# Performance work log

Measured on AMD Instinct MI355X. Metric: run time of the kernel, lower is better.

## Reference

```python
import jax, jax.numpy as jnp
import numpy as np

B, N, IN_DIM, HID, OUT_DIM = 16, 1024, 128, 256, 1024
N_LAYERS, SCT_ORDER, GCN_ORDER = 2, 3, 1
TAU, N_ITER, NOISE_SCALE, TANH_SCALE = 0.1, 20, 0.05, 40.0


def _xavier(key, shape):
    # torch xavier_uniform_ on Linear weight [out, in]
    bound = np.sqrt(6.0 / (shape[-1] + shape[-2]))
    return jax.random.uniform(key, shape, jnp.float32, -bound, bound)


def setup_inputs() -> dict:
    key = jax.random.key(0)
    ks = jax.random.split(key, 12)
    L, H = N_LAYERS, HID
    return {
        "X": jax.random.normal(ks[0], (B, N, IN_DIM), jnp.float32),
        "adj": jax.random.uniform(ks[1], (B, N, N), jnp.float32),
        "w_in": _xavier(ks[2], (H, IN_DIM)),
        "b_in": jnp.zeros((H,), jnp.float32),
        "conv_w1": _xavier(ks[3], (L, H, H)),
        "conv_b1": jnp.zeros((L, H), jnp.float32),
        "conv_w2": _xavier(ks[4], (L, H, H)),
        "conv_b2": jnp.zeros((L, H), jnp.float32),
        "conv_a": 0.1 * jax.random.normal(ks[5], (L, 2 * H, 1), jnp.float32),
        "mlp1_w": _xavier(ks[6], (H, H * (1 + L))),
        "mlp1_b": jnp.zeros((H,), jnp.float32),
        "mlp2_w": _xavier(ks[7], (OUT_DIM, H)),
        "mlp2_b": jnp.zeros((OUT_DIM,), jnp.float32),
    }


def leaky(x):
    return jax.nn.leaky_relu(x, 0.01)


def gcn_diffusion(adj, order, X):
    eye = jnp.eye(adj.shape[-1], dtype=adj.dtype)
    A = adj + eye
    dis = A.sum(-1) ** -0.5                      # [B,N]
    A_hat = dis[..., :, None] * A * dis[..., None, :]
    outs, h = [], X
    for _ in range(order):
        h = A_hat @ h
        outs.append(h)
    return outs


def scattering_diffusion(adj, X, order):
    # lazy random walk P = (I + D^{-1} A)/2; wavelets psi_k = P^{2^{k-1}} - P^{2^k}
    Pmat = adj / adj.sum(-1, keepdims=True)

    def applyP(h):
        return 0.5 * (h + Pmat @ h)

    outs = []
    prev = X
    cur = applyP(X)
    outs.append(prev - cur)
    for k in range(2, order + 1):
        nxt = cur
        for _ in range(2 ** (k - 2)):
            nxt = applyP(nxt)
        outs.append(cur - nxt)
        cur = nxt
    return outs


def sct_conv(X, adj, w1, b1, w2, b2, a, moment=1):
    gcn_list = [leaky(g) for g in gcn_diffusion(adj, GCN_ORDER, X)]
    sct_list = [jnp.abs(h) ** moment for h in scattering_diffusion(adj, X, SCT_ORDER)]
    h_all = jnp.stack(gcn_list + sct_list, axis=1)                    # [B,C,N,H]
    x_rep = jnp.broadcast_to(X[:, None], h_all.shape)                 # [B,C,N,H]
    a_in = jnp.concatenate([x_rep, h_all], axis=-1)                   # [B,C,N,2H]
    e = (jax.nn.relu(a_in) @ a)[..., 0]                               # [B,C,N]
    attention = jax.nn.softmax(e + 1e-10, axis=1)[..., None]          # [B,C,N,1]
    h_prime = (attention * h_all).mean(axis=1)                        # [B,N,H]
    h = leaky(h_prime @ w1.T + b1)
    return leaky(h @ w2.T + b2)


def gumbel_sinkhorn(log_alpha, key):
    u = jax.random.uniform(key, log_alpha.shape, log_alpha.dtype)
    noise = -jnp.log(-jnp.log(u + 1e-20) + 1e-20) * NOISE_SCALE
    Z0 = (log_alpha + noise) / TAU

    def step(Z, _):
        Z = Z - jax.scipy.special.logsumexp(Z, axis=-1, keepdims=True)
        Z = Z - jax.scipy.special.logsumexp(Z, axis=-2, keepdims=True)
        return Z, None

    Z, _ = jax.lax.scan(step, Z0, None, length=N_ITER)
    P = jnp.exp(Z)
    P = P / P.sum(-1, keepdims=True)
    P = P / P.sum(-2, keepdims=True)
    return P, Z0


def reference(X, adj, w_in, b_in, conv_w1, conv_b1, conv_w2, conv_b2, conv_a,
              mlp1_w, mlp1_b, mlp2_w, mlp2_b):
    h = X @ w_in.T + b_in                                             # [B,N,H]
    hidden = [h]
    for l in range(N_LAYERS):
        h = sct_conv(h, adj, conv_w1[l], conv_b1[l], conv_w2[l], conv_b2[l], conv_a[l])
        hidden.append(h)
    h = jnp.concatenate(hidden, axis=-1)                              # [B,N,H*(1+L)]
    h = leaky(h @ mlp1_w.T + mlp1_b)
    logits = jnp.tanh(h @ mlp2_w.T + mlp2_b) * TANH_SCALE             # [B,N,N]
    P, gsinit = gumbel_sinkhorn(logits, jax.random.key(42))
    return P, gsinit
```

## Files before the change

### kernel.cpp

```cpp
#include <hip/hip_runtime.h>
#include <cstdint>
#include <cstddef>

#define BB 16
#define NN 1024
#define HD 256
#define IND 128
#define OUTD 1024
#define MROWS (BB*NN)

#define LEAKY(x) ((x) >= 0.0f ? (x) : 0.01f*(x))

typedef short short8 __attribute__((ext_vector_type(8)));
typedef float f32x4 __attribute__((ext_vector_type(4)));

#define GLL16(gsrc, ldst) __builtin_amdgcn_global_load_lds( \
    (const __attribute__((address_space(1))) unsigned int*)(gsrc), \
    (__attribute__((address_space(3))) unsigned int*)(ldst), 16, 0, 0)

__device__ inline float wave_sum(float v){
  #pragma unroll
  for (int off=32; off; off>>=1) v += __shfl_xor(v, off, 64);
  return v;
}
__device__ inline float wave_max(float v){
  #pragma unroll
  for (int off=32; off; off>>=1) v = fmaxf(v, __shfl_xor(v, off, 64));
  return v;
}

__device__ inline unsigned short f2bf(float x){
  unsigned u = __float_as_uint(x);
  unsigned r = (u + 0x7fffu + ((u >> 16) & 1u)) >> 16;
  return (unsigned short)r;
}
__device__ inline float bf2f(unsigned short h){
  return __uint_as_float((unsigned)h << 16);
}

__device__ inline float gumbel_noise(unsigned m){
  const unsigned k0 = 0u, k1 = 42u;
  const unsigned ks2 = k0 ^ k1 ^ 0x1BD11BDAu;
  unsigned x0 = 0u, x1 = m;
  x0 += k0; x1 += k1;
  #define TF_ROUND(r) { x0 += x1; x1 = (x1 << (r)) | (x1 >> (32-(r))); x1 ^= x0; }
  TF_ROUND(13) TF_ROUND(15) TF_ROUND(26) TF_ROUND(6)
  x0 += k1;  x1 += ks2 + 1u;
  TF_ROUND(17) TF_ROUND(29) TF_ROUND(16) TF_ROUND(24)
  x0 += ks2; x1 += k0 + 2u;
  TF_ROUND(13) TF_ROUND(15) TF_ROUND(26) TF_ROUND(6)
  x0 += k0;  x1 += k1 + 3u;
  TF_ROUND(17) TF_ROUND(29) TF_ROUND(16) TF_ROUND(24)
  x0 += k1;  x1 += ks2 + 4u;
  TF_ROUND(13) TF_ROUND(15) TF_ROUND(26) TF_ROUND(6)
  x0 += ks2; x1 += k0 + 5u;
  #undef TF_ROUND
  unsigned bits = x0 ^ x1;
  float u = __uint_as_float((bits >> 9) | 0x3f800000u) - 1.0f;
  float t = -__logf(u + 1e-20f);
  return -__logf(t + 1e-20f) * 0.05f;
}

__global__ __launch_bounds__(256) void adj_prep_k(const float* __restrict__ adj,
                                                  float* __restrict__ dis,
                                                  float* __restrict__ rinv,
                                                  unsigned short* __restrict__ abf){
  int tid = threadIdx.x, wid = tid >> 6, lane = tid & 63;
  int row = blockIdx.x*4 + wid;
  const float4* rp = (const float4*)(adj + (size_t)row*NN);
  ushort4* op = (ushort4*)(abf + (size_t)row*NN);
  float s = 0.f;
  #pragma unroll
  for (int p=0;p<4;p++){
    float4 v = rp[lane + p*64];
    s += v.x+v.y+v.z+v.w;
    ushort4 o;
    o.x = f2bf(v.x); o.y = f2bf(v.y); o.z = f2bf(v.z); o.w = f2bf(v.w);
    op[lane + p*64] = o;
  }
  s = wave_sum(s);
  if (lane==0){
    dis[row]  = 1.0f/sqrtf(s + 1.0f);
    rinv[row] = 1.0f/s;
  }
}

__global__ __launch_bounds__(256) void split_flat_k(const float* __restrict__ src,
                                                    unsigned short* __restrict__ h,
                                                    unsigned short* __restrict__ l,
                                                    int n4){
  int gid = blockIdx.x*256 + threadIdx.x;
  if (gid >= n4) return;
  float4 v = ((const float4*)src)[gid];
  ushort4 hh, ll;
  hh.x = f2bf(v.x); ll.x = f2bf(v.x - bf2f(hh.x));
  hh.y = f2bf(v.y); ll.y = f2bf(v.y - bf2f(hh.y));
  hh.z = f2bf(v.z); ll.z = f2bf(v.z - bf2f(hh.z));
  hh.w = f2bf(v.w); ll.w = f2bf(v.w - bf2f(hh.w));
  ((ushort4*)h)[gid] = hh;
  ((ushort4*)l)[gid] = ll;
}

__global__ __launch_bounds__(256) void bconv_t_k(const float* __restrict__ in, int ld,
                                                 const float* __restrict__ scale,
                                                 unsigned short* __restrict__ outT){
  __shared__ float tile[64][68];
  int b  = blockIdx.z;
  int i0 = blockIdx.x*64;
  int c0 = blockIdx.y*64;
  const float* inb = in + (size_t)b*NN*ld;
  unsigned short* ob = outT + (size_t)b*HD*NN;
  int tid = threadIdx.x;
  #pragma unroll
  for (int it=0; it<4; it++){
    int f = tid + it*256;
    int r = f >> 4, c4 = (f & 15)*4;
    float4 v = *(const float4*)(inb + (size_t)(i0+r)*ld + c0 + c4);
    float s = scale ? scale[b*NN + i0 + r] : 1.0f;
    tile[r][c4+0]=v.x*s; tile[r][c4+1]=v.y*s; tile[r][c4+2]=v.z*s; tile[r][c4+3]=v.w*s;
  }
  __syncthreads();
  #pragma unroll
  for (int it=0; it<4; it++){
    int f = tid + it*256;
    int cl = f >> 4, r4 = (f & 15)*4;
    ushort4 o;
    o.x = f2bf(tile[r4+0][cl]);
    o.y = f2bf(tile[r4+1][cl]);
    o.z = f2bf(tile[r4+2][cl]);
    o.w = f2bf(tile[r4+3][cl]);
    *(ushort4*)(ob + (size_t)(c0+cl)*NN + i0 + r4) = o;
  }
}

__global__ __launch_bounds__(512) void gemm_nn_mfma_k(const unsigned short* __restrict__ Abf,
                                                      const unsigned short* __restrict__ Btb,
                                                      const float* __restrict__ Bsrc, int ldb,
                                                      const float* __restrict__ rowscale,
                                                      float* __restrict__ out,
                                                      float* __restrict__ out2,
                                                      const float* __restrict__ sub,
                                                      int mode){
  __shared__ unsigned short Als[128][32];
  __shared__ unsigned short Bls[128][32];
  int b  = blockIdx.z;
  int n0 = blockIdx.x*128;
  int i0 = blockIdx.y*128;
  const unsigned short* Ab = Abf + (size_t)b*NN*NN + (size_t)i0*NN;
  const unsigned short* Bb = Btb + (size_t)b*HD*NN + (size_t)n0*NN;
  int tid = threadIdx.x;
  int wave = tid >> 6, lane = tid & 63;
  int quad = lane >> 4, l16 = lane & 15;
  int wr = (wave >> 2)*64;
  int wc = (wave & 3)*32;

  int r  = tid >> 2;
  int cg = (((tid & 3) ^ ((r >> 1) & 3)) << 3);
  int wbase = (tid >> 6) << 9;
  unsigned short* lA = &Als[0][0] + wbase;
  unsigned short* lB = &Bls[0][0] + wbase;
  const unsigned short* gA = Ab + (size_t)r*NN + cg;
  const unsigned short* gB = Bb + (size_t)r*NN + cg;

  f32x4 acc[4][2] = {};

  for (int kc = 0; kc < NN; kc += 32){
    GLL16(gA + kc, lA);
    GLL16(gB + kc, lB);
    __syncthreads();
    short8 af[4];
    #pragma unroll
    for (int rt=0; rt<4; rt++){
      int R = wr + rt*16 + l16;
      af[rt] = *(const short8*)&Als[R][(quad ^ ((R >> 1) & 3)) << 3];
    }
    #pragma unroll
    for (int ct=0; ct<2; ct++){
      int Rb = wc + ct*16 + l16;
      short8 bfr = *(const short8*)&Bls[Rb][(quad ^ ((Rb >> 1) & 3)) << 3];
      #pragma unroll
      for (int rt=0; rt<4; rt++)
        acc[rt][ct] = __builtin_amdgcn_mfma_f32_16x16x32_bf16(af[rt], bfr, acc[rt][ct], 0, 0, 0);
    }
    __syncthreads();
  }

  #pragma unroll
  for (int rt=0; rt<4; rt++){
    #pragma unroll
    for (int p=0; p<4; p++){
      int gr = i0 + wr + rt*16 + quad*4 + p;
      int gm = b*NN + gr;
      float sc = rowscale[gm];
      #pragma unroll
      for (int ct=0; ct<2; ct++){
        int gc = n0 + wc + ct*16 + l16;
        float a = acc[rt][ct][p];
        float src = Bsrc[(size_t)gm*ldb + gc];
        float o = (mode == 1) ? 0.5f*(src + sc*a) : LEAKY(sc*(a + sc*src));
        if (out) out[(size_t)gm*HD + gc] = o;
        if (out2){
          float sv = sub ? sub[(size_t)gm*HD + gc] : src;
          out2[(size_t)gm*HD + gc] = fabsf(sv - o);
        }
      }
    }
  }
}

__global__ __launch_bounds__(512) void gemm_nt_mfma_k(const float* __restrict__ Ain,
                                                      const unsigned short* __restrict__ Ah_,
                                                      const unsigned short* __restrict__ Al_,
                                                      int lda,
                                                      const unsigned short* __restrict__ Wh_,
                                                      const unsigned short* __restrict__ Wl_,
                                                      const float* __restrict__ bias,
                                                      float* __restrict__ out, int ldo,
                                                      unsigned short* __restrict__ outh,
                                                      unsigned short* __restrict__ outl,
                                                      int K, int act){
  __shared__ unsigned short Ah[128][32], Al[128][32], Bh[128][32], Bl[128][32];
  int o0 = blockIdx.x*128, m0 = blockIdx.y*128;
  int tid = threadIdx.x;
  int wave = tid >> 6, lane = tid & 63;
  int quad = lane >> 4, l16 = lane & 15;
  int wr = (wave >> 2)*64;
  int wc = (wave & 3)*32;

  int r  = tid >> 2;
  int cg = (((tid & 3) ^ ((r >> 1) & 3)) << 3);
  int wbase = (tid >> 6) << 9;
  unsigned short* lAh = &Ah[0][0] + wbase;
  unsigned short* lAl = &Al[0][0] + wbase;
  unsigned short* lBh = &Bh[0][0] + wbase;
  unsigned short* lBl = &Bl[0][0] + wbase;
  const unsigned short* gWh = Wh_ + (size_t)(o0 + r)*K + cg;
  const unsigned short* gWl = Wl_ + (size_t)(o0 + r)*K + cg;
  const unsigned short* gAh = Ah_ ? Ah_ + (size_t)(m0 + r)*lda + cg : (const unsigned short*)0;
  const unsigned short* gAl = Ah_ ? Al_ + (size_t)(m0 + r)*lda + cg : (const unsigned short*)0;

  f32x4 acc[4][2] = {};

  for (int kc = 0; kc < K; kc += 32){
    GLL16(gWh + kc, lBh);
    GLL16(gWl + kc, lBl);
    if (Ah_){
      GLL16(gAh + kc, lAh);
      GLL16(gAl + kc, lAl);
    } else {
      #pragma unroll
      for (int it=0; it<2; it++){
        int f = tid + it*512;
        int rr = f >> 3, c4 = (f & 7)*4;
        float4 va = *(const float4*)(Ain + (size_t)(m0+rr)*lda + kc + c4);
        ushort4 h, lo;
        h.x = f2bf(va.x); lo.x = f2bf(va.x - bf2f(h.x));
        h.y = f2bf(va.y); lo.y = f2bf(va.y - bf2f(h.y));
        h.z = f2bf(va.z); lo.z = f2bf(va.z - bf2f(h.z));
        h.w = f2bf(va.w); lo.w = f2bf(va.w - bf2f(h.w));
        int sw = (((c4 >> 3) ^ ((rr >> 1) & 3)) << 3) | (c4 & 7);
        *(ushort4*)&Ah[rr][sw] = h;
        *(ushort4*)&Al[rr][sw] = lo;
      }
    }
    __syncthreads();
    short8 ahv[4], alv[4];
    #pragma unroll
    for (int rt=0; rt<4; rt++){
      int R = wr + rt*16 + l16;
      int sc = (quad ^ ((R >> 1) & 3)) << 3;
      ahv[rt] = *(const short8*)&Ah[R][sc];
      alv[rt] = *(const short8*)&Al[R][sc];
    }
    #pragma unroll
    for (int ct=0; ct<2; ct++){
      int Rb = wc + ct*16 + l16;
      int sc = (quad ^ ((Rb >> 1) & 3)) << 3;
      short8 bh = *(const short8*)&Bh[Rb][sc];
      short8 bl = *(const short8*)&Bl[Rb][sc];
      #pragma unroll
      for (int rt=0; rt<4; rt++){
        acc[rt][ct] = __builtin_amdgcn_mfma_f32_16x16x32_bf16(ahv[rt], bh, acc[rt][ct], 0, 0, 0);
        acc[rt][ct] = __builtin_amdgcn_mfma_f32_16x16x32_bf16(alv[rt], bh, acc[rt][ct], 0, 0, 0);
        acc[rt][ct] = __builtin_amdgcn_mfma_f32_16x16x32_bf16(ahv[rt], bl, acc[rt][ct], 0, 0, 0);
      }
    }
    __syncthreads();
  }

  #pragma unroll
  for (int rt=0; rt<4; rt++){
    #pragma unroll
    for (int p=0; p<4; p++){
      int gm = m0 + wr + rt*16 + quad*4 + p;
      #pragma unroll
      for (int ct=0; ct<2; ct++){
        int gc = o0 + wc + ct*16 + l16;
        float v = acc[rt][ct][p] + bias[gc];
        if (act == 1){
          v = LEAKY(v);
        } else if (act == 2){
          float vcl = fminf(fmaxf(v, -15.f), 15.f);
          float e = __expf(2.f*vcl);
          float lg = 40.0f * (e - 1.f) / (e + 1.f);
          unsigned flat = (unsigned)gm*1024u + (unsigned)gc;
          v = (lg + gumbel_noise(flat)) / 0.1f;
        }
        if (out) out[(size_t)gm*ldo + gc] = v;
        if (outh){
          unsigned short hh = f2bf(v);
          outh[(size_t)gm*ldo + gc] = hh;
          outl[(size_t)gm*ldo + gc] = f2bf(v - bf2f(hh));
        }
      }
    }
  }
}

__global__ __launch_bounds__(256) void attn_k(const float* __restrict__ c0,
                                              const float* __restrict__ s0,
                                              const float* __restrict__ s1,
                                              const float* __restrict__ s2,
                                              const float* __restrict__ a2,
                                              unsigned short* __restrict__ outh,
                                              unsigned short* __restrict__ outl){
  int tid = threadIdx.x, wid = tid >> 6, lane = tid & 63;
  int row = blockIdx.x*4 + wid;
  size_t base = (size_t)row*HD + lane*4;
  float4 av = *(const float4*)(a2 + lane*4);
  float4 v[4];
  v[0] = *(const float4*)(c0 + base);
  v[1] = *(const float4*)(s0 + base);
  v[2] = *(const float4*)(s1 + base);
  v[3] = *(const float4*)(s2 + base);
  float e[4];
  #pragma unroll
  for (int c=0;c<4;c++){
    float p = fmaxf(v[c].x,0.f)*av.x + fmaxf(v[c].y,0.f)*av.y
            + fmaxf(v[c].z,0.f)*av.z + fmaxf(v[c].w,0.f)*av.w;
    e[c] = wave_sum(p);
  }
  float m = fmaxf(fmaxf(e[0],e[1]), fmaxf(e[2],e[3]));
  float w0 = expf(e[0]-m), w1 = expf(e[1]-m), w2 = expf(e[2]-m), w3 = expf(e[3]-m);
  float inv = 0.25f / (w0+w1+w2+w3);
  float4 o;
  o.x = (w0*v[0].x + w1*v[1].x + w2*v[2].x + w3*v[3].x)*inv;
  o.y = (w0*v[0].y + w1*v[1].y + w2*v[2].y + w3*v[3].y)*inv;
  o.z = (w0*v[0].z + w1*v[1].z + w2*v[2].z + w3*v[3].z)*inv;
  o.w = (w0*v[0].w + w1*v[1].w + w2*v[2].w + w3*v[3].w)*inv;
  ushort4 oh, ol;
  oh.x = f2bf(o.x); ol.x = f2bf(o.x - bf2f(oh.x));
  oh.y = f2bf(o.y); ol.y = f2bf(o.y - bf2f(oh.y));
  oh.z = f2bf(o.z); ol.z = f2bf(o.z - bf2f(oh.z));
  oh.w = f2bf(o.w); ol.w = f2bf(o.w - bf2f(oh.w));
  *(ushort4*)(outh + base) = oh;
  *(ushort4*)(outl + base) = ol;
}


__global__ __launch_bounds__(256) void rowmax_k(const float* __restrict__ Z,
                                                float* __restrict__ alpha){
  int tid = threadIdx.x, wid = tid >> 6, lane = tid & 63;
  int row = blockIdx.x*4 + wid;
  const float4* rp = (const float4*)(Z + (size_t)row*NN);
  float m = -3.4e38f;
  #pragma unroll
  for (int p=0;p<4;p++){
    float4 v = rp[lane + p*64];
    m = fmaxf(m, fmaxf(fmaxf(v.x,v.y), fmaxf(v.z,v.w)));
  }
  m = wave_max(m);
  if (lane==0) alpha[row] = m;
}

__global__ __launch_bounds__(256) void colmax_k(const float* __restrict__ Z,
                                                const float* __restrict__ alpha,
                                                float* __restrict__ pmax){
  int b = blockIdx.y, rc = blockIdx.x;
  int j = threadIdx.x*4;
  const float* Zb = Z + (size_t)b*NN*NN;
  const float* ab = alpha + b*NN;
  float4 m = make_float4(-3.4e38f,-3.4e38f,-3.4e38f,-3.4e38f);
  int r0 = rc*32;
  #pragma unroll 4
  for (int r=r0; r<r0+32; r++){
    float4 v = *(const float4*)(Zb + (size_t)r*NN + j);
    float a = ab[r];
    m.x = fmaxf(m.x, v.x-a); m.y = fmaxf(m.y, v.y-a);
    m.z = fmaxf(m.z, v.z-a); m.w = fmaxf(m.w, v.w-a);
  }
  *(float4*)(pmax + ((size_t)b*32 + rc)*NN + j) = m;
}

__global__ __launch_bounds__(256) void colred_k(const float* __restrict__ pmax,
                                                float* __restrict__ beta){
  int b = blockIdx.y;
  int j = blockIdx.x*256 + threadIdx.x;
  float m = -3.4e38f;
  #pragma unroll
  for (int rc=0; rc<32; rc++)
    m = fmaxf(m, pmax[((size_t)b*32+rc)*NN + j]);
  beta[b*NN + j] = m;
}

__global__ __launch_bounds__(256) void build_e_k(const float* __restrict__ Z,
                                                 const float* __restrict__ alpha,
                                                 const float* __restrict__ beta,
                                                 unsigned short* __restrict__ E,
                                                 unsigned short* __restrict__ Et){
  __shared__ float tile[64][65];
  int b = blockIdx.z;
  int i0 = blockIdx.y*64, j0 = blockIdx.x*64;
  const float* Zb = Z + (size_t)b*NN*NN;
  const float* ab = alpha + b*NN;
  const float* bb = beta  + b*NN;
  unsigned short* Eb  = E  + (size_t)b*NN*NN;
  unsigned short* Etb = Et + (size_t)b*NN*NN;
  int tid = threadIdx.x;
  #pragma unroll
  for (int it=0; it<4; it++){
    int f = tid + it*256;
    int r = f >> 4, c4 = (f & 15)*4;
    float4 v = *(const float4*)(Zb + (size_t)(i0+r)*NN + j0 + c4);
    float a = ab[i0+r];
    float e0 = __expf(v.x - a - bb[j0+c4+0]);
    float e1 = __expf(v.y - a - bb[j0+c4+1]);
    float e2 = __expf(v.z - a - bb[j0+c4+2]);
    float e3 = __expf(v.w - a - bb[j0+c4+3]);
    tile[r][c4+0]=e0; tile[r][c4+1]=e1; tile[r][c4+2]=e2; tile[r][c4+3]=e3;
    ushort4 o; o.x=f2bf(e0); o.y=f2bf(e1); o.z=f2bf(e2); o.w=f2bf(e3);
    *(ushort4*)(Eb + (size_t)(i0+r)*NN + j0 + c4) = o;
  }
  __syncthreads();
  #pragma unroll
  for (int it=0; it<4; it++){
    int f = tid + it*256;
    int r = f >> 4, c4 = (f & 15)*4;
    ushort4 o;
    o.x = f2bf(tile[c4+0][r]);
    o.y = f2bf(tile[c4+1][r]);
    o.z = f2bf(tile[c4+2][r]);
    o.w = f2bf(tile[c4+3][r]);
    *(ushort4*)(Etb + (size_t)(j0+r)*NN + i0 + c4) = o;
  }
}

__global__ __launch_bounds__(256) void mv_k(const unsigned short* __restrict__ M,
                                            const float* __restrict__ v,
                                            float* __restrict__ w, int recip){
  int tid = threadIdx.x, wid = tid >> 6, lane = tid & 63;
  int row = blockIdx.x*4 + wid;
  int b = row >> 10;
  const unsigned short* mp = M + (size_t)row*NN + lane*16;
  float s = 0.f;
  if (v){
    const float* vb = v + b*NN + lane*16;
    #pragma unroll
    for (int h2=0; h2<2; h2++){
      short8 m8 = *(const short8*)(mp + h2*8);
      float4 v0 = *(const float4*)(vb + h2*8);
      float4 v1 = *(const float4*)(vb + h2*8 + 4);
      s += bf2f((unsigned short)m8[0])*v0.x + bf2f((unsigned short)m8[1])*v0.y
         + bf2f((unsigned short)m8[2])*v0.z + bf2f((unsigned short)m8[3])*v0.w
         + bf2f((unsigned short)m8[4])*v1.x + bf2f((unsigned short)m8[5])*v1.y
         + bf2f((unsigned short)m8[6])*v1.z + bf2f((unsigned short)m8[7])*v1.w;
    }
  } else {
    #pragma unroll
    for (int h2=0; h2<2; h2++){
      short8 m8 = *(const short8*)(mp + h2*8);
      #pragma unroll
      for (int q=0;q<8;q++) s += bf2f((unsigned short)m8[q]);
    }
  }
  s = wave_sum(s);
  if (lane==0) w[row] = recip ? 1.0f/s : s;
}

__global__ __launch_bounds__(256) void writep_lin_k(const unsigned short* __restrict__ E,
                                                    const float* __restrict__ ap,
                                                    const float* __restrict__ tp,
                                                    float* __restrict__ P){
  int gid = blockIdx.x*256 + threadIdx.x;
  int row = gid >> 8;
  int j = (gid & 255)*4;
  int b = row >> 10;
  ushort4 e = ((const ushort4*)E)[gid];
  float a = ap[row];
  float4 t = *(const float4*)(tp + (size_t)b*NN + j);
  float4 o;
  o.x = bf2f(e.x)*a/t.x;
  o.y = bf2f(e.y)*a/t.y;
  o.z = bf2f(e.z)*a/t.z;
  o.w = bf2f(e.w)*a/t.w;
  ((float4*)P)[gid] = o;
}

extern "C" void kernel_launch(void* const* d_in, const int* in_sizes, int n_in,
                              void* d_out, int out_size, void* d_ws, size_t ws_size,
                              hipStream_t stream){
  const float* X    = (const float*)d_in[0];
  const float* adj  = (const float*)d_in[1];
  const float* w_in = (const float*)d_in[2];
  const float* b_in = (const float*)d_in[3];
  const float* cw1  = (const float*)d_in[4];
  const float* cb1  = (const float*)d_in[5];
  const float* cw2  = (const float*)d_in[6];
  const float* cb2  = (const float*)d_in[7];
  const float* ca   = (const float*)d_in[8];
  const float* m1w  = (const float*)d_in[9];
  const float* m1b  = (const float*)d_in[10];
  const float* m2w  = (const float*)d_in[11];
  const float* m2b  = (const float*)d_in[12];

  float* outp = (float*)d_out;
  float* Pout = outp;
  float* Z0   = outp + (size_t)16*1024*1024;

  const size_t SLOT = (size_t)4*1024*1024;
  float* s1 = outp + 0*SLOT;
  float* s2 = outp + 1*SLOT;
  float* s3 = outp + 2*SLOT;
  float* s4 = outp + 3*SLOT;
  float* s5 = outp + 4*SLOT;
  float* s6 = outp + 5*SLOT;
  unsigned short* adjbf = (unsigned short*)(outp + 6*SLOT);

  unsigned short* Xh  = (unsigned short*)(outp + 0*SLOT);
  unsigned short* Xl  = Xh + (size_t)MROWS*IND;
  unsigned short* s4h = (unsigned short*)(outp + 3*SLOT);
  unsigned short* s4l = s4h + (size_t)MROWS*HD;
  unsigned short* l1h = (unsigned short*)(outp + 0*SLOT);
  unsigned short* l1l = l1h + (size_t)MROWS*HD;
  unsigned short* m1sh = (unsigned short*)(outp + 1*SLOT);
  unsigned short* m1sl = m1sh + (size_t)MROWS*HD;
  float* alpha = s1;
  float* beta  = s1 + 16384;
  float* pmaxb = s1 + 32768;

  float* ws     = (float*)d_ws;
  float* hidden = ws;
  float* dis    = ws + (size_t)12*1024*1024;
  float* rinv   = dis + 16384;
  unsigned short* bt = (unsigned short*)(rinv + 16384);
  unsigned short* wsp = (unsigned short*)(ws + (size_t)15*1024*1024);
  unsigned short* winh = wsp;               unsigned short* winl = winh + 32768;
  unsigned short* w1h  = winl + 32768;      unsigned short* w1l  = w1h + 131072;
  unsigned short* w2h  = w1l + 131072;      unsigned short* w2l  = w2h + 131072;
  unsigned short* m1h  = w2l + 131072;      unsigned short* m1l  = m1h + 196608;
  unsigned short* m2h  = m1l + 196608;      unsigned short* m2l  = m2h + 262144;
  unsigned short* E  = (unsigned short*)ws;
  unsigned short* Et = E + (size_t)MROWS*NN;
  float* av = ws + (size_t)16*1024*1024;
  float* bv = av + 16384;
  float* tv = bv + 16384;

  dim3 blk(256);
  dim3 gEw(4096);
  dim3 gMM(2, 8, 16);
  dim3 gCT(16, 4, 16);

  adj_prep_k<<<gEw, blk, 0, stream>>>(adj, dis, rinv, adjbf);
  split_flat_k<<<dim3(32),  blk, 0, stream>>>(w_in, winh, winl, 8192);
  split_flat_k<<<dim3(128), blk, 0, stream>>>(cw1,  w1h,  w1l,  32768);
  split_flat_k<<<dim3(128), blk, 0, stream>>>(cw2,  w2h,  w2l,  32768);
  split_flat_k<<<dim3(192), blk, 0, stream>>>(m1w,  m1h,  m1l,  49152);
  split_flat_k<<<dim3(256), blk, 0, stream>>>(m2w,  m2h,  m2l,  65536);
  split_flat_k<<<dim3(2048), blk, 0, stream>>>(X, Xh, Xl, 524288);

  gemm_nt_mfma_k<<<dim3(2,128), dim3(512), 0, stream>>>(nullptr, Xh, Xl, IND,
                                                        winh, winl, b_in,
                                                        hidden, 768, nullptr, nullptr,
                                                        IND, 0);

  for (int l=0; l<2; l++){
    const float* h_in = hidden + l*HD;
    unsigned short* wl1h = w1h + (size_t)l*65536;
    unsigned short* wl1l = w1l + (size_t)l*65536;
    unsigned short* wl2h = w2h + (size_t)l*65536;
    unsigned short* wl2l = w2l + (size_t)l*65536;
    const float* b1 = cb1 + (size_t)l*HD;
    const float* b2 = cb2 + (size_t)l*HD;
    const float* a2 = ca  + (size_t)l*2*HD + HD;

    bconv_t_k<<<gCT, blk, 0, stream>>>(h_in, 768, dis, bt);
    gemm_nn_mfma_k<<<gMM, dim3(512), 0, stream>>>(adjbf, bt, h_in, 768, dis, s2, nullptr, nullptr, 2);
    bconv_t_k<<<gCT, blk, 0, stream>>>(h_in, 768, nullptr, bt);
    gemm_nn_mfma_k<<<gMM, dim3(512), 0, stream>>>(adjbf, bt, h_in, 768, rinv, s1, s3, nullptr, 1);
    bconv_t_k<<<gCT, blk, 0, stream>>>(s1, HD, nullptr, bt);
    gemm_nn_mfma_k<<<gMM, dim3(512), 0, stream>>>(adjbf, bt, s1, HD, rinv, s4, s5, nullptr, 1);
    bconv_t_k<<<gCT, blk, 0, stream>>>(s4, HD, nullptr, bt);
    gemm_nn_mfma_k<<<gMM, dim3(512), 0, stream>>>(adjbf, bt, s4, HD, rinv, s1, nullptr, nullptr, 1);
    bconv_t_k<<<gCT, blk, 0, stream>>>(s1, HD, nullptr, bt);
    gemm_nn_mfma_k<<<gMM, dim3(512), 0, stream>>>(adjbf, bt, s1, HD, rinv, nullptr, s1, s4, 1);
    attn_k<<<gEw, blk, 0, stream>>>(s2, s3, s5, s1, a2, s4h, s4l);
    gemm_nt_mfma_k<<<dim3(2,128), dim3(512), 0, stream>>>(nullptr, s4h, s4l, HD,
                                                          wl1h, wl1l, b1,
                                                          nullptr, HD, l1h, l1l,
                                                          HD, 1);
    gemm_nt_mfma_k<<<dim3(2,128), dim3(512), 0, stream>>>(nullptr, l1h, l1l, HD,
                                                          wl2h, wl2l, b2,
                                                          hidden + (l+1)*HD, 768,
                                                          nullptr, nullptr, HD, 1);
  }

  gemm_nt_mfma_k<<<dim3(2,128), dim3(512), 0, stream>>>(hidden, nullptr, nullptr, 768,
                                                        m1h, m1l, m1b,
                                                        nullptr, HD, m1sh, m1sl,
                                                        768, 1);
  gemm_nt_mfma_k<<<dim3(8,128), dim3(512), 0, stream>>>(nullptr, m1sh, m1sl, HD,
                                                        m2h, m2l, m2b,
                                                        Z0, OUTD, nullptr, nullptr,
                                                        HD, 2);

  rowmax_k<<<gEw, blk, 0, stream>>>(Z0, alpha);
  colmax_k<<<dim3(32,16), blk, 0, stream>>>(Z0, alpha, pmaxb);
  colred_k<<<dim3(4,16), blk, 0, stream>>>(pmaxb, beta);
  build_e_k<<<dim3(16,16,16), blk, 0, stream>>>(Z0, alpha, beta, E, Et);

  mv_k<<<gEw, blk, 0, stream>>>(E,  nullptr, av, 1);
  mv_k<<<gEw, blk, 0, stream>>>(Et, av,      bv, 1);
  for (int t=1; t<20; t++){
    mv_k<<<gEw, blk, 0, stream>>>(E,  bv, av, 1);
    mv_k<<<gEw, blk, 0, stream>>>(Et, av, bv, 1);
  }
  mv_k<<<gEw, blk, 0, stream>>>(E,  bv, av, 1);
  mv_k<<<gEw, blk, 0, stream>>>(Et, av, tv, 0);
  writep_lin_k<<<dim3(16384), blk, 0, stream>>>(E, av, tv, Pout);
}
```

Measured before the change: 1.208 ms.

## Multi-buffer GEMM K-loops with async LDS prefetch and split-bf16 passes

Both MFMA GEMM kernels now use a 4-slot LDS ring filled by global_load_lds two tiles ahead. A manual vmcnt wait plus a single barrier replaces the two __syncthreads per step, and setprio is raised around the MFMA block. The NT GEMM is restructured so the three split-bf16 products (hi*hi, lo*hi, hi*lo) run as three sequential K passes through one A/W buffer pair, which cuts LDS footprint and per-step register use. The fp32 hidden input path is replaced by a separate split kernel, so in-kernel conversion goes away at the cost of an extra pass over the 768-wide activations. There is a risk of LDS buffer reuse races, since a slot is refilled two steps later with only one barrier between reads and overwrites.

```diff
diff --git a/kernel.cpp b/kernel.cpp
--- a/kernel.cpp
+++ b/kernel.cpp
@@ -17,6 +17,8 @@
 #define GLL16(gsrc, ldst) __builtin_amdgcn_global_load_lds( \
     (const __attribute__((address_space(1))) unsigned int*)(gsrc), \
     (__attribute__((address_space(3))) unsigned int*)(ldst), 16, 0, 0)
+
+#define CFENCE() asm volatile("" ::: "memory")
 
 __device__ inline float wave_sum(float v){
   #pragma unroll
@@ -141,8 +143,8 @@
                                                       float* __restrict__ out2,
                                                       const float* __restrict__ sub,
                                                       int mode){
-  __shared__ unsigned short Als[128][32];
-  __shared__ unsigned short Bls[128][32];
+  __shared__ unsigned short Als[4][128][32];
+  __shared__ unsigned short Bls[4][128][32];
   int b  = blockIdx.z;
   int n0 = blockIdx.x*128;
   int i0 = blockIdx.y*128;
@@ -157,32 +159,48 @@
   int r  = tid >> 2;
   int cg = (((tid & 3) ^ ((r >> 1) & 3)) << 3);
   int wbase = (tid >> 6) << 9;
-  unsigned short* lA = &Als[0][0] + wbase;
-  unsigned short* lB = &Bls[0][0] + wbase;
   const unsigned short* gA = Ab + (size_t)r*NN + cg;
   const unsigned short* gB = Bb + (size_t)r*NN + cg;
 
+  auto STAGE = [&](int tt){
+    int buf = tt & 3;
+    GLL16(gA + tt*32, &Als[buf][0][0] + wbase);
+    GLL16(gB + tt*32, &Bls[buf][0][0] + wbase);
+  };
+
+  const int NT = NN/32;
+  STAGE(0); STAGE(1);
+
   f32x4 acc[4][2] = {};
 
-  for (int kc = 0; kc < NN; kc += 32){
-    GLL16(gA + kc, lA);
-    GLL16(gB + kc, lB);
-    __syncthreads();
+  for (int t = 0; t < NT; ++t){
+    if (t+2 < NT){
+      STAGE(t+2);
+      asm volatile("s_waitcnt vmcnt(4)" ::: "memory");
+    } else if (t+1 < NT){
+      asm volatile("s_waitcnt vmcnt(2)" ::: "memory");
+    } else {
+      asm volatile("s_waitcnt vmcnt(0)" ::: "memory");
+    }
+    __builtin_amdgcn_s_barrier();
+    CFENCE();
+    int buf = t & 3;
     short8 af[4];
     #pragma unroll
     for (int rt=0; rt<4; rt++){
       int R = wr + rt*16 + l16;
-      af[rt] = *(const short8*)&Als[R][(quad ^ ((R >> 1) & 3)) << 3];
-    }
+      af[rt] = *(const short8*)&Als[buf][R][(quad ^ ((R >> 1) & 3)) << 3];
+    }
+    __builtin_amdgcn_s_setprio(1);
     #pragma unroll
     for (int ct=0; ct<2; ct++){
       int Rb = wc + ct*16 + l16;
-      short8 bfr = *(const short8*)&Bls[Rb][(quad ^ ((Rb >> 1) & 3)) << 3];
+      short8 bfr = *(const short8*)&Bls[buf][Rb][(quad ^ ((Rb >> 1) & 3)) << 3];
       #pragma unroll
       for (int rt=0; rt<4; rt++)
         acc[rt][ct] = __builtin_amdgcn_mfma_f32_16x16x32_bf16(af[rt], bfr, acc[rt][ct], 0, 0, 0);
     }
-    __syncthreads();
+    __builtin_amdgcn_s_setprio(0);
   }
 
   #pragma unroll
@@ -208,8 +226,7 @@
   }
 }
 
-__global__ __launch_bounds__(512) void gemm_nt_mfma_k(const float* __restrict__ Ain,
-                                                      const unsigned short* __restrict__ Ah_,
+__global__ __launch_bounds__(512) void gemm_nt_mfma_k(const unsigned short* __restrict__ Ah_,
                                                       const unsigned short* __restrict__ Al_,
                                                       int lda,
                                                       const unsigned short* __restrict__ Wh_,
@@ -219,7 +236,8 @@
                                                       unsigned short* __restrict__ outh,
                                                       unsigned short* __restrict__ outl,
                                                       int K, int act){
-  __shared__ unsigned short Ah[128][32], Al[128][32], Bh[128][32], Bl[128][32];
+  __shared__ unsigned short Alds[4][128][32];
+  __shared__ unsigned short Wlds[4][128][32];
   int o0 = blockIdx.x*128, m0 = blockIdx.y*128;
   int tid = threadIdx.x;
   int wave = tid >> 6, lane = tid & 63;
@@ -230,62 +248,56 @@
   int r  = tid >> 2;
   int cg = (((tid & 3) ^ ((r >> 1) & 3)) << 3);
   int wbase = (tid >> 6) << 9;
-  unsigned short* lAh = &Ah[0][0] + wbase;
-  unsigned short* lAl = &Al[0][0] + wbase;
-  unsigned short* lBh = &Bh[0][0] + wbase;
-  unsigned short* lBl = &Bl[0][0] + wbase;
+  const unsigned short* gAh = Ah_ + (size_t)(m0 + r)*lda + cg;
+  const unsigned short* gAl = Al_ + (size_t)(m0 + r)*lda + cg;
   const unsigned short* gWh = Wh_ + (size_t)(o0 + r)*K + cg;
   const unsigned short* gWl = Wl_ + (size_t)(o0 + r)*K + cg;
-  const unsigned short* gAh = Ah_ ? Ah_ + (size_t)(m0 + r)*lda + cg : (const unsigned short*)0;
-  const unsigned short* gAl = Ah_ ? Al_ + (size_t)(m0 + r)*lda + cg : (const unsigned short*)0;
+
+  int nk = K >> 5;
+  int NT = 3*nk;
+
+  auto STAGE = [&](int tt){
+    int buf = tt & 3;
+    const unsigned short* sa; const unsigned short* sw; int kc;
+    if (tt < nk)        { sa = gAh; sw = gWh; kc = tt << 5; }
+    else if (tt < 2*nk) { sa = gAl; sw = gWh; kc = (tt - nk) << 5; }
+    else                { sa = gAh; sw = gWl; kc = (tt - 2*nk) << 5; }
+    GLL16(sa + kc, &Alds[buf][0][0] + wbase);
+    GLL16(sw + kc, &Wlds[buf][0][0] + wbase);
+  };
+
+  STAGE(0); STAGE(1);
 
   f32x4 acc[4][2] = {};
 
-  for (int kc = 0; kc < K; kc += 32){
-    GLL16(gWh + kc, lBh);
-    GLL16(gWl + kc, lBl);
-    if (Ah_){
-      GLL16(gAh + kc, lAh);
-      GLL16(gAl + kc, lAl);
+  for (int t = 0; t < NT; ++t){
+    if (t+2 < NT){
+      STAGE(t+2);
+      asm volatile("s_waitcnt vmcnt(4)" ::: "memory");
+    } else if (t+1 < NT){
+      asm volatile("s_waitcnt vmcnt(2)" ::: "memory");
     } else {
-      #pragma unroll
-      for (int it=0; it<2; it++){
-        int f = tid + it*512;
-        int rr = f >> 3, c4 = (f & 7)*4;
-        float4 va = *(const float4*)(Ain + (size_t)(m0+rr)*lda + kc + c4);
-        ushort4 h, lo;
-        h.x = f2bf(va.x); lo.x = f2bf(va.x - bf2f(h.x));
-        h.y = f2bf(va.y); lo.y = f2bf(va.y - bf2f(h.y));
-        h.z = f2bf(va.z); lo.z = f2bf(va.z - bf2f(h.z));
-        h.w = f2bf(va.w); lo.w = f2bf(va.w - bf2f(h.w));
-        int sw = (((c4 >> 3) ^ ((rr >> 1) & 3)) << 3) | (c4 & 7);
-        *(ushort4*)&Ah[rr][sw] = h;
-        *(ushort4*)&Al[rr][sw] = lo;
-      }
-    }
-    __syncthreads();
-    short8 ahv[4], alv[4];
+      asm volatile("s_waitcnt vmcnt(0)" ::: "memory");
+    }
+    __builtin_amdgcn_s_barrier();
+    CFENCE();
+    int buf = t & 3;
+    short8 af[4];
     #pragma unroll
     for (int rt=0; rt<4; rt++){
       int R = wr + rt*16 + l16;
-      int sc = (quad ^ ((R >> 1) & 3)) << 3;
-      ahv[rt] = *(const short8*)&Ah[R][sc];
-      alv[rt] = *(const short8*)&Al[R][sc];
-    }
+      af[rt] = *(const short8*)&Alds[buf][R][(quad ^ ((R >> 1) & 3)) << 3];
+    }
+    __builtin_amdgcn_s_setprio(1);
     #pragma unroll
     for (int ct=0; ct<2; ct++){
       int Rb = wc + ct*16 + l16;
-      int sc = (quad ^ ((Rb >> 1) & 3)) << 3;
-      short8 bh = *(const short8*)&Bh[Rb][sc];
-      short8 bl = *(const short8*)&Bl[Rb][sc];
+      short8 bfr = *(const short8*)&Wlds[buf][Rb][(quad ^ ((Rb >> 1) & 3)) << 3];
       #pragma unroll
-      for (int rt=0; rt<4; rt++){
-        acc[rt][ct] = __builtin_amdgcn_mfma_f32_16x16x32_bf16(ahv[rt], bh, acc[rt][ct], 0, 0, 0);
-        acc[rt][ct] = __builtin_amdgcn_mfma_f32_16x16x32_bf16(alv[rt], bh, acc[rt][ct], 0, 0, 0);
-        acc[rt][ct] = __builtin_amdgcn_mfma_f32_16x16x32_bf16(ahv[rt], bl, acc[rt][ct], 0, 0, 0);
-      }
-    }
-    __syncthreads();
+      for (int rt=0; rt<4; rt++)
+        acc[rt][ct] = __builtin_amdgcn_mfma_f32_16x16x32_bf16(af[rt], bfr, acc[rt][ct], 0, 0, 0);
+    }
+    __builtin_amdgcn_s_setprio(0);
   }
 
   #pragma unroll
@@ -357,7 +369,6 @@
   *(ushort4*)(outl + base) = ol;
 }
 
-
 __global__ __launch_bounds__(256) void rowmax_k(const float* __restrict__ Z,
                                                 float* __restrict__ alpha){
   int tid = threadIdx.x, wid = tid >> 6, lane = tid & 63;
@@ -523,7 +534,6 @@
   float* s3 = outp + 2*SLOT;
   float* s4 = outp + 3*SLOT;
   float* s5 = outp + 4*SLOT;
-  float* s6 = outp + 5*SLOT;
   unsigned short* adjbf = (unsigned short*)(outp + 6*SLOT);
 
   unsigned short* Xh  = (unsigned short*)(outp + 0*SLOT);
@@ -534,6 +544,8 @@
   unsigned short* l1l = l1h + (size_t)MROWS*HD;
   unsigned short* m1sh = (unsigned short*)(outp + 1*SLOT);
   unsigned short* m1sl = m1sh + (size_t)MROWS*HD;
+  unsigned short* Hh = (unsigned short*)(outp + 2*SLOT);
+  unsigned short* Hl = Hh + (size_t)MROWS*768;
   float* alpha = s1;
   float* beta  = s1 + 16384;
   float* pmaxb = s1 + 32768;
@@ -568,7 +580,7 @@
   split_flat_k<<<dim3(256), blk, 0, stream>>>(m2w,  m2h,  m2l,  65536);
   split_flat_k<<<dim3(2048), blk, 0, stream>>>(X, Xh, Xl, 524288);
 
-  gemm_nt_mfma_k<<<dim3(2,128), dim3(512), 0, stream>>>(nullptr, Xh, Xl, IND,
+  gemm_nt_mfma_k<<<dim3(2,128), dim3(512), 0, stream>>>(Xh, Xl, IND,
                                                         winh, winl, b_in,
                                                         hidden, 768, nullptr, nullptr,
                                                         IND, 0);
@@ -594,21 +606,22 @@
     bconv_t_k<<<gCT, blk, 0, stream>>>(s1, HD, nullptr, bt);
     gemm_nn_mfma_k<<<gMM, dim3(512), 0, stream>>>(adjbf, bt, s1, HD, rinv, nullptr, s1, s4, 1);
     attn_k<<<gEw, blk, 0, stream>>>(s2, s3, s5, s1, a2, s4h, s4l);
-    gemm_nt_mfma_k<<<dim3(2,128), dim3(512), 0, stream>>>(nullptr, s4h, s4l, HD,
+    gemm_nt_mfma_k<<<dim3(2,128), dim3(512), 0, stream>>>(s4h, s4l, HD,
                                                           wl1h, wl1l, b1,
                                                           nullptr, HD, l1h, l1l,
                                                           HD, 1);
-    gemm_nt_mfma_k<<<dim3(2,128), dim3(512), 0, stream>>>(nullptr, l1h, l1l, HD,
+    gemm_nt_mfma_k<<<dim3(2,128), dim3(512), 0, stream>>>(l1h, l1l, HD,
                                                           wl2h, wl2l, b2,
                                                           hidden + (l+1)*HD, 768,
                                                           nullptr, nullptr, HD, 1);
   }
 
-  gemm_nt_mfma_k<<<dim3(2,128), dim3(512), 0, stream>>>(hidden, nullptr, nullptr, 768,
+  split_flat_k<<<dim3(12288), blk, 0, stream>>>(hidden, Hh, Hl, 3145728);
+  gemm_nt_mfma_k<<<dim3(2,128), dim3(512), 0, stream>>>(Hh, Hl, 768,
                                                         m1h, m1l, m1b,
                                                         nullptr, HD, m1sh, m1sl,
                                                         768, 1);
-  gemm_nt_mfma_k<<<dim3(8,128), dim3(512), 0, stream>>>(nullptr, m1sh, m1sl, HD,
+  gemm_nt_mfma_k<<<dim3(8,128), dim3(512), 0, stream>>>(m1sh, m1sl, HD,
                                                         m2h, m2l, m2b,
                                                         Z0, OUTD, nullptr, nullptr,
                                                         HD, 2);
```

New measurement: 1.202 ms. About the same (-0.5%).
